# Optimization experiments

Measured on AMD Instinct MI355X. Metric: run time of the kernel, lower is better.

The kernel has to match this reference:

```python
import jax, jax.numpy as jnp
import numpy as np

V, D, H, E, C, K = 16000, 1024, 1024, 8, 16, 2  # vocab, embed, expert hidden, n_experts, classes, top_k
B, S = 64, 512
GATE_H = 256


def setup_inputs() -> dict:
    key = jax.random.key(0)
    ks = jax.random.split(key, 11)
    s = lambda i, shape: jax.random.normal(ks[i], shape, jnp.float32) * 0.02
    return dict(
        x=jax.random.randint(ks[0], (B, S), 0, V),
        emb=s(1, (V, D)),                      # shared gating embedding
        gate_w1=s(2, (D, GATE_H)), gate_b1=jnp.zeros((GATE_H,), jnp.float32),
        gate_w2=s(3, (GATE_H, E)), gate_b2=jnp.zeros((E,), jnp.float32),
        exp_emb=s(4, (E, V, D)),               # per-expert embedding tables
        exp_w1=s(5, (E, D, H)), exp_b1=jnp.zeros((E, H), jnp.float32),
        exp_w2=s(6, (E, H, C)), exp_b2=jnp.zeros((E, C), jnp.float32),
    )


def reference(x, emb, gate_w1, gate_b1, gate_w2, gate_b2,
              exp_emb, exp_w1, exp_b1, exp_w2, exp_b2):
    # --- gating: embed, mean-pool over seq, 2-layer MLP, softmax, top-k ---
    pooled = emb[x].mean(axis=1)                                   # [B,D]
    logits = jax.nn.relu(pooled @ gate_w1 + gate_b1) @ gate_w2 + gate_b2  # [B,E]
    probs = jax.nn.softmax(logits, axis=-1)
    rw, idx = jax.lax.top_k(probs, K)                              # [B,K]
    rw = rw / rw.sum(axis=-1, keepdims=True)                       # renormalize

    # --- dispatch: gather each sample's assigned expert params (no per-sample loop) ---
    out = jnp.zeros((x.shape[0], C), jnp.float32)
    for k in range(K):  # tiny fixed loop over top_k
        e = idx[:, k]                                              # [B]
        tok = exp_emb[e[:, None], x]                               # [B,S,D]
        h = jax.nn.relu(jnp.einsum('bsd,bdh->bsh', tok, exp_w1[e]) + exp_b1[e][:, None, :])  # [B,S,H]
        p = h.mean(axis=1)                                         # [B,H]
        eo = jnp.einsum('bh,bhc->bc', p, exp_w2[e]) + exp_b2[e]    # [B,C]
        out = out + rw[:, k:k + 1] * eo
    return out
```

## Files before the change

kernel.cpp:

```cpp
#include <hip/hip_runtime.h>
#include <hip/hip_bf16.h>

#define V_   16000
#define D_   1024
#define H_   1024
#define E_   8
#define C_   16
#define B_   64
#define S_   512
#define GH_  256
#define NPAIR 128

typedef short  bf16x8 __attribute__((ext_vector_type(8)));
typedef ushort u16x8  __attribute__((ext_vector_type(8)));
typedef float  f32x4  __attribute__((ext_vector_type(4)));

static __device__ __forceinline__ ushort f2bf(float f) {
  union { float f; unsigned u; } un; un.f = f;
  unsigned u = un.u;
  return (ushort)((u + 0x7FFFu + ((u >> 16) & 1u)) >> 16);
}

static __device__ __forceinline__ unsigned pk2(float lo, float hi) {
  __hip_bfloat162 h = __float22bfloat162_rn(make_float2(lo, hi));
  unsigned r; __builtin_memcpy(&r, &h, sizeof(r)); return r;
}

__global__ void prep_kernel(const float* __restrict__ w1, ushort* __restrict__ w1t,
                            const int* __restrict__ x, const float* __restrict__ emb,
                            float* __restrict__ partial) {
  __shared__ float tile[64][65];
  const int id = blockIdx.x;
  if (id < 2048) {
    const int e = id >> 8, rem = id & 255;
    const int dtile = rem & 15, htile = rem >> 4;
    const int d0 = dtile * 64, h0 = htile * 64;
    const float* src = w1 + (size_t)e * D_ * H_;
    for (int i = threadIdx.x; i < 64 * 64; i += 256) {
      int r = i >> 6, c = i & 63;
      tile[r][c] = src[(size_t)(d0 + r) * H_ + h0 + c];
    }
    __syncthreads();
    for (int i = threadIdx.x; i < 512; i += 256) {
      int chunk = i >> 6, lane = i & 63;
      int kkl = chunk >> 2, htl = chunk & 3;
      int l15 = lane & 15, l16 = lane >> 4;
      u16x8 v;
      #pragma unroll
      for (int j = 0; j < 8; ++j)
        v[j] = f2bf(tile[kkl * 32 + l16 * 8 + j][htl * 16 + l15]);
      size_t off = ((size_t)((e * 32 + dtile * 2 + kkl) * 64 + htile * 4 + htl)) * 512 + lane * 8;
      *reinterpret_cast<u16x8*>(w1t + off) = v;
    }
  } else {
    const int pid = id - 2048;
    const int b = pid >> 3, sb = pid & 7, t = threadIdx.x;
    const int* xr = x + b * S_ + sb * 64;
    float4 acc = make_float4(0.f, 0.f, 0.f, 0.f);
    #pragma unroll 4
    for (int s = 0; s < 64; ++s) {
      const float4* row = reinterpret_cast<const float4*>(emb + (size_t)xr[s] * D_);
      float4 v = row[t];
      acc.x += v.x; acc.y += v.y; acc.z += v.z; acc.w += v.w;
    }
    reinterpret_cast<float4*>(partial + ((size_t)b * 8 + sb) * D_)[t] = acc;
  }
}

__global__ void gate_kernel(const float* __restrict__ partial,
                            const float* __restrict__ gw1, const float* __restrict__ gb1,
                            const float* __restrict__ gw2, const float* __restrict__ gb2,
                            int* __restrict__ ridx, float* __restrict__ rwgt) {
  const int b = blockIdx.x, j = threadIdx.x;
  __shared__ float pl[D_];
  __shared__ float hid[GH_];
  __shared__ float logits[E_];
  for (int d = j; d < D_; d += 256) {
    float s = 0.f;
    #pragma unroll
    for (int sb = 0; sb < 8; ++sb) s += partial[((size_t)b * 8 + sb) * D_ + d];
    pl[d] = s * (1.f / (float)S_);
  }
  __syncthreads();
  float acc = gb1[j];
  for (int d = 0; d < D_; ++d) acc += pl[d] * gw1[d * GH_ + j];
  hid[j] = fmaxf(acc, 0.f);
  __syncthreads();
  if (j < E_) {
    float l = gb2[j];
    for (int i = 0; i < GH_; ++i) l += hid[i] * gw2[i * E_ + j];
    logits[j] = l;
  }
  __syncthreads();
  if (j == 0) {
    int i0 = 0; float v0 = logits[0];
    for (int i = 1; i < E_; ++i) if (logits[i] > v0) { v0 = logits[i]; i0 = i; }
    int i1 = -1; float v1 = -3.0e38f;
    for (int i = 0; i < E_; ++i) {
      if (i == i0) continue;
      if (logits[i] > v1) { v1 = logits[i]; i1 = i; }
    }
    float r1 = expf(v1 - v0);
    float norm = 1.f + r1;
    ridx[b * 2 + 0] = i0;         ridx[b * 2 + 1] = i1;
    rwgt[b * 2 + 0] = 1.f / norm; rwgt[b * 2 + 1] = r1 / norm;
  }
}

__global__ void sort_pairs_kernel(const int* __restrict__ ridx, int* __restrict__ order) {
  __shared__ int se[NPAIR];
  const int t = threadIdx.x;
  se[t] = ridx[t];
  __syncthreads();
  const int e = se[t];
  int rank = 0;
  for (int j = 0; j < NPAIR; ++j) {
    const int ej = se[j];
    rank += (ej < e || (ej == e && j < t)) ? 1 : 0;
  }
  order[rank] = t;
}

__global__ __launch_bounds__(512, 2) void expert_kernel(
    const int* __restrict__ x, const float* __restrict__ exp_emb,
    const ushort* __restrict__ w1t, const float* __restrict__ exp_b1,
    const int* __restrict__ ridx, const int* __restrict__ order,
    float* __restrict__ p_part) {
  const int id     = blockIdx.x;
  const int xcd    = id & 7;
  const int within = id >> 3;
  const int slot   = xcd * 128 + within;
  const int pr     = order[slot >> 3];
  const int sblk   = slot & 7;
  const int b      = pr >> 1;
  const int tid    = threadIdx.x;

  __shared__ __align__(16) ushort lB[64 * 1024];

  const int e = ridx[pr];

  const int grow = tid >> 3, gkq = (tid & 7) * 8;
  const int tok  = x[b * S_ + sblk * 64 + grow];
  const float* gptr = exp_emb + ((size_t)e * V_ + tok) * D_ + gkq;
  const int gdst = grow * 1024 + (gkq ^ ((grow & 7) << 3));

  const int wid = tid >> 6, lane = tid & 63;
  const int l15 = lane & 15, l16 = lane >> 4;
  const int sw  = (l15 & 7) << 3;

  const ushort* aW = w1t + (size_t)e * (32 * 64 * 512) + ((size_t)wid * 4) * 512 + (size_t)lane * 8;
  #define LOADA(t_, i_) \
    (*reinterpret_cast<const bf16x8*>(aW + ((size_t)(((t_) & 31) * 64 + ((t_) >> 5) * 32 + (i_))) * 512))

  f32x4 acc[4][4];
  #pragma unroll
  for (int i = 0; i < 4; ++i)
    #pragma unroll
    for (int j = 0; j < 4; ++j) acc[i][j] = (f32x4){0.f, 0.f, 0.f, 0.f};

  {
    f32x4 c0 = __builtin_nontemporal_load(reinterpret_cast<const f32x4*>(gptr));
    f32x4 c1 = __builtin_nontemporal_load(reinterpret_cast<const f32x4*>(gptr + 4));
    uint4 w;
    w.x = pk2(c0[0], c0[1]); w.y = pk2(c0[2], c0[3]);
    w.z = pk2(c1[0], c1[1]); w.w = pk2(c1[2], c1[3]);
    *reinterpret_cast<uint4*>(&lB[gdst]) = w;
  }

  bf16x8 af[4];
  #pragma unroll
  for (int i = 0; i < 4; ++i) af[i] = LOADA(0, i);

  #pragma unroll
  for (int slab = 0; slab < 16; ++slab) {
    __syncthreads();
    f32x4 n0, n1;
    if (slab < 15) {
      n0 = __builtin_nontemporal_load(reinterpret_cast<const f32x4*>(gptr + (slab + 1) * 64));
      n1 = __builtin_nontemporal_load(reinterpret_cast<const f32x4*>(gptr + (slab + 1) * 64 + 4));
    }
    #pragma unroll
    for (int ks = 0; ks < 2; ++ks) {
      const int kk = slab * 2 + ks;
      bf16x8 afn[4];
      #pragma unroll
      for (int i = 0; i < 4; ++i) afn[i] = LOADA(kk + 1, i);
      const int colk = (kk >> 1) * 64 + ((((kk & 1) << 5) | (l16 << 3)) ^ sw);
      bf16x8 bfr[4];
      #pragma unroll
      for (int j = 0; j < 4; ++j)
        bfr[j] = *reinterpret_cast<const bf16x8*>(&lB[(j * 16 + l15) * 1024 + colk]);
      #pragma unroll
      for (int i = 0; i < 4; ++i)
        #pragma unroll
        for (int j = 0; j < 4; ++j)
          acc[i][j] = __builtin_amdgcn_mfma_f32_16x16x32_bf16(af[i], bfr[j], acc[i][j], 0, 0, 0);
      #pragma unroll
      for (int i = 0; i < 4; ++i) af[i] = afn[i];
    }
    if (slab < 15) {
      uint4 w;
      w.x = pk2(n0[0], n0[1]); w.y = pk2(n0[2], n0[3]);
      w.z = pk2(n1[0], n1[1]); w.w = pk2(n1[2], n1[3]);
      *reinterpret_cast<uint4*>(&lB[gdst + (slab + 1) * 64]) = w;
    }
  }

  float* outRow = p_part + (size_t)(sblk * NPAIR + pr) * H_;
  const float* biasE = exp_b1 + e * H_;
  #pragma unroll
  for (int i = 0; i < 4; ++i) {
    #pragma unroll
    for (int r = 0; r < 4; ++r) {
      const int h = wid * 64 + i * 16 + l16 * 4 + r;
      const float bias = biasE[h];
      float v = 0.f;
      #pragma unroll
      for (int j = 0; j < 4; ++j) v += fmaxf(acc[i][j][r] + bias, 0.f);
      #pragma unroll
      for (int m = 1; m < 16; m <<= 1) v += __shfl_xor(v, m);
      if (l15 == 0) outRow[h] = v;
      acc[i][0][r] = 0.f;
    }
    #pragma unroll
    for (int j = 1; j < 4; ++j) acc[i][j] = (f32x4){0.f, 0.f, 0.f, 0.f};
  }

  #pragma unroll 4
  for (int t2 = 32; t2 < 64; ++t2) {
    bf16x8 afn[4];
    if (t2 < 63) {
      #pragma unroll
      for (int i = 0; i < 4; ++i) afn[i] = LOADA(t2 + 1, i);
    }
    const int kk = t2 - 32;
    const int colk = (kk >> 1) * 64 + ((((kk & 1) << 5) | (l16 << 3)) ^ sw);
    bf16x8 bfr[4];
    #pragma unroll
    for (int j = 0; j < 4; ++j)
      bfr[j] = *reinterpret_cast<const bf16x8*>(&lB[(j * 16 + l15) * 1024 + colk]);
    #pragma unroll
    for (int i = 0; i < 4; ++i)
      #pragma unroll
      for (int j = 0; j < 4; ++j)
        acc[i][j] = __builtin_amdgcn_mfma_f32_16x16x32_bf16(af[i], bfr[j], acc[i][j], 0, 0, 0);
    #pragma unroll
    for (int i = 0; i < 4; ++i) af[i] = afn[i];
  }

  #pragma unroll
  for (int i = 0; i < 4; ++i) {
    #pragma unroll
    for (int r = 0; r < 4; ++r) {
      const int h = 512 + wid * 64 + i * 16 + l16 * 4 + r;
      const float bias = biasE[h];
      float v = 0.f;
      #pragma unroll
      for (int j = 0; j < 4; ++j) v += fmaxf(acc[i][j][r] + bias, 0.f);
      #pragma unroll
      for (int m = 1; m < 16; m <<= 1) v += __shfl_xor(v, m);
      if (l15 == 0) outRow[h] = v;
    }
  }
  #undef LOADA
}

__global__ void finalize_kernel(const float* __restrict__ p_part,
                                const int* __restrict__ ridx, const float* __restrict__ rwgt,
                                const float* __restrict__ w2, const float* __restrict__ b2,
                                float* __restrict__ out) {
  const int b = blockIdx.x, t = threadIdx.x;
  const int c = t & 15, g = t >> 4;
  __shared__ float red[16][17];
  float res = 0.f;
  for (int kk = 0; kk < 2; ++kk) {
    const int pr = b * 2 + kk;
    const int e = ridx[pr];
    const float w = rwgt[pr];
    float dot = 0.f;
    for (int h = g; h < H_; h += 16) {
      float pm = 0.f;
      #pragma unroll
      for (int sb = 0; sb < 8; ++sb) pm += p_part[(size_t)(sb * NPAIR + pr) * H_ + h];
      dot += pm * w2[((size_t)e * H_ + h) * C_ + c];
    }
    red[g][c] = dot;
    __syncthreads();
    if (g == 0) {
      float s = 0.f;
      #pragma unroll
      for (int i = 0; i < 16; ++i) s += red[i][c];
      res += w * (s * (1.f / (float)S_) + b2[e * C_ + c]);
    }
    __syncthreads();
  }
  if (g == 0) out[b * C_ + c] = res;
}

extern "C" void kernel_launch(void* const* d_in, const int* in_sizes, int n_in,
                              void* d_out, int out_size, void* d_ws, size_t ws_size,
                              hipStream_t stream) {
  const int*   x    = (const int*)  d_in[0];
  const float* emb  = (const float*)d_in[1];
  const float* gw1  = (const float*)d_in[2];
  const float* gb1  = (const float*)d_in[3];
  const float* gw2  = (const float*)d_in[4];
  const float* gb2  = (const float*)d_in[5];
  const float* eemb = (const float*)d_in[6];
  const float* ew1  = (const float*)d_in[7];
  const float* eb1  = (const float*)d_in[8];
  const float* ew2  = (const float*)d_in[9];
  const float* eb2  = (const float*)d_in[10];
  float* out = (float*)d_out;

  char* ws = (char*)d_ws;
  const size_t OFF_W1T   = 0;
  const size_t OFF_PART  = (size_t)16 << 20;
  const size_t OFF_RIDX  = OFF_PART + ((size_t)2 << 20);
  const size_t OFF_RWGT  = OFF_RIDX + 1024;
  const size_t OFF_ORDER = OFF_RWGT + 1024;
  const size_t OFF_PPART = OFF_ORDER + 1024;

  ushort* w1t    = (ushort*)(ws + OFF_W1T);
  float*  part   = (float*) (ws + OFF_PART);
  int*    ridx   = (int*)   (ws + OFF_RIDX);
  float*  rwgt   = (float*) (ws + OFF_RWGT);
  int*    order  = (int*)   (ws + OFF_ORDER);
  float*  ppart  = (float*) (ws + OFF_PPART);

  prep_kernel<<<dim3(2560), 256, 0, stream>>>(ew1, w1t, x, emb, part);
  gate_kernel<<<dim3(B_), 256, 0, stream>>>(part, gw1, gb1, gw2, gb2, ridx, rwgt);
  sort_pairs_kernel<<<dim3(1), 128, 0, stream>>>(ridx, order);
  expert_kernel<<<dim3(1024), 512, 0, stream>>>(x, eemb, w1t, eb1, ridx, order, ppart);
  finalize_kernel<<<dim3(B_), 256, 0, stream>>>(ppart, ridx, rwgt, ew2, eb2, out);
}
```

Measured before the change: 301.6 us.

## Fuse both H halves into one K pass with 3-deep gather prefetch

The expert GEMM now processes both 512-wide H halves in a single sweep over K, keeping two accumulator sets (128 fp32 acc registers). The embedding gather is prefetched three slabs ahead in registers instead of one, and the barrier is replaced with an explicit lgkmcnt wait plus s_barrier placed after the LDS write. The aim is to overlap more of the global gather latency and remove the second LDS read pass over the tile. The cost is much higher register pressure, which may cut occupancy or cause spills, and the A-operand loads are no longer software-prefetched one step ahead.

```diff
diff --git a/kernel.cpp b/kernel.cpp
--- a/kernel.cpp
+++ b/kernel.cpp
@@ -24,6 +24,11 @@
 static __device__ __forceinline__ unsigned pk2(float lo, float hi) {
   __hip_bfloat162 h = __float22bfloat162_rn(make_float2(lo, hi));
   unsigned r; __builtin_memcpy(&r, &h, sizeof(r)); return r;
+}
+
+static __device__ __forceinline__ void bar_lgkm() {
+  asm volatile("s_waitcnt lgkmcnt(0)" ::: "memory");
+  __builtin_amdgcn_s_barrier();
 }
 
 __global__ void prep_kernel(const float* __restrict__ w1, ushort* __restrict__ w1t,
@@ -149,117 +154,86 @@
   const int sw  = (l15 & 7) << 3;
 
   const ushort* aW = w1t + (size_t)e * (32 * 64 * 512) + ((size_t)wid * 4) * 512 + (size_t)lane * 8;
-  #define LOADA(t_, i_) \
-    (*reinterpret_cast<const bf16x8*>(aW + ((size_t)(((t_) & 31) * 64 + ((t_) >> 5) * 32 + (i_))) * 512))
-
-  f32x4 acc[4][4];
+  #define LOADA(kk_, hh_, i_) \
+    (*reinterpret_cast<const bf16x8*>(aW + ((size_t)((kk_) * 64 + (hh_) * 32 + (i_))) * 512))
+
+  f32x4 acc[2][4][4];
   #pragma unroll
-  for (int i = 0; i < 4; ++i)
+  for (int hh = 0; hh < 2; ++hh)
     #pragma unroll
-    for (int j = 0; j < 4; ++j) acc[i][j] = (f32x4){0.f, 0.f, 0.f, 0.f};
-
+    for (int i = 0; i < 4; ++i)
+      #pragma unroll
+      for (int j = 0; j < 4; ++j) acc[hh][i][j] = (f32x4){0.f, 0.f, 0.f, 0.f};
+
+  f32x4 st[3][2];
+  #pragma unroll
+  for (int p = 0; p < 3; ++p) {
+    st[p][0] = __builtin_nontemporal_load(reinterpret_cast<const f32x4*>(gptr + p * 64));
+    st[p][1] = __builtin_nontemporal_load(reinterpret_cast<const f32x4*>(gptr + p * 64 + 4));
+  }
   {
-    f32x4 c0 = __builtin_nontemporal_load(reinterpret_cast<const f32x4*>(gptr));
-    f32x4 c1 = __builtin_nontemporal_load(reinterpret_cast<const f32x4*>(gptr + 4));
     uint4 w;
-    w.x = pk2(c0[0], c0[1]); w.y = pk2(c0[2], c0[3]);
-    w.z = pk2(c1[0], c1[1]); w.w = pk2(c1[2], c1[3]);
+    w.x = pk2(st[0][0][0], st[0][0][1]); w.y = pk2(st[0][0][2], st[0][0][3]);
+    w.z = pk2(st[0][1][0], st[0][1][1]); w.w = pk2(st[0][1][2], st[0][1][3]);
     *reinterpret_cast<uint4*>(&lB[gdst]) = w;
   }
-
-  bf16x8 af[4];
+  bar_lgkm();
+
   #pragma unroll
-  for (int i = 0; i < 4; ++i) af[i] = LOADA(0, i);
-
-  #pragma unroll
-  for (int slab = 0; slab < 16; ++slab) {
-    __syncthreads();
-    f32x4 n0, n1;
-    if (slab < 15) {
-      n0 = __builtin_nontemporal_load(reinterpret_cast<const f32x4*>(gptr + (slab + 1) * 64));
-      n1 = __builtin_nontemporal_load(reinterpret_cast<const f32x4*>(gptr + (slab + 1) * 64 + 4));
+  for (int s = 0; s < 16; ++s) {
+    if (s + 3 < 16) {
+      st[s % 3][0] = __builtin_nontemporal_load(reinterpret_cast<const f32x4*>(gptr + (s + 3) * 64));
+      st[s % 3][1] = __builtin_nontemporal_load(reinterpret_cast<const f32x4*>(gptr + (s + 3) * 64 + 4));
     }
     #pragma unroll
     for (int ks = 0; ks < 2; ++ks) {
-      const int kk = slab * 2 + ks;
-      bf16x8 afn[4];
-      #pragma unroll
-      for (int i = 0; i < 4; ++i) afn[i] = LOADA(kk + 1, i);
-      const int colk = (kk >> 1) * 64 + ((((kk & 1) << 5) | (l16 << 3)) ^ sw);
+      const int kk = s * 2 + ks;
+      const int colk = s * 64 + (((ks << 5) | (l16 << 3)) ^ sw);
       bf16x8 bfr[4];
       #pragma unroll
       for (int j = 0; j < 4; ++j)
         bfr[j] = *reinterpret_cast<const bf16x8*>(&lB[(j * 16 + l15) * 1024 + colk]);
+      bf16x8 af0[4], af1[4];
+      #pragma unroll
+      for (int i = 0; i < 4; ++i) { af0[i] = LOADA(kk, 0, i); af1[i] = LOADA(kk, 1, i); }
       #pragma unroll
       for (int i = 0; i < 4; ++i)
         #pragma unroll
         for (int j = 0; j < 4; ++j)
-          acc[i][j] = __builtin_amdgcn_mfma_f32_16x16x32_bf16(af[i], bfr[j], acc[i][j], 0, 0, 0);
-      #pragma unroll
-      for (int i = 0; i < 4; ++i) af[i] = afn[i];
-    }
-    if (slab < 15) {
+          acc[0][i][j] = __builtin_amdgcn_mfma_f32_16x16x32_bf16(af0[i], bfr[j], acc[0][i][j], 0, 0, 0);
+      #pragma unroll
+      for (int i = 0; i < 4; ++i)
+        #pragma unroll
+        for (int j = 0; j < 4; ++j)
+          acc[1][i][j] = __builtin_amdgcn_mfma_f32_16x16x32_bf16(af1[i], bfr[j], acc[1][i][j], 0, 0, 0);
+    }
+    if (s + 1 < 16) {
+      const int p = (s + 1) % 3;
       uint4 w;
-      w.x = pk2(n0[0], n0[1]); w.y = pk2(n0[2], n0[3]);
-      w.z = pk2(n1[0], n1[1]); w.w = pk2(n1[2], n1[3]);
-      *reinterpret_cast<uint4*>(&lB[gdst + (slab + 1) * 64]) = w;
-    }
+      w.x = pk2(st[p][0][0], st[p][0][1]); w.y = pk2(st[p][0][2], st[p][0][3]);
+      w.z = pk2(st[p][1][0], st[p][1][1]); w.w = pk2(st[p][1][2], st[p][1][3]);
+      *reinterpret_cast<uint4*>(&lB[gdst + (s + 1) * 64]) = w;
+    }
+    bar_lgkm();
   }
 
   float* outRow = p_part + (size_t)(sblk * NPAIR + pr) * H_;
   const float* biasE = exp_b1 + e * H_;
   #pragma unroll
-  for (int i = 0; i < 4; ++i) {
+  for (int hh = 0; hh < 2; ++hh) {
     #pragma unroll
-    for (int r = 0; r < 4; ++r) {
-      const int h = wid * 64 + i * 16 + l16 * 4 + r;
-      const float bias = biasE[h];
-      float v = 0.f;
-      #pragma unroll
-      for (int j = 0; j < 4; ++j) v += fmaxf(acc[i][j][r] + bias, 0.f);
-      #pragma unroll
-      for (int m = 1; m < 16; m <<= 1) v += __shfl_xor(v, m);
-      if (l15 == 0) outRow[h] = v;
-      acc[i][0][r] = 0.f;
-    }
-    #pragma unroll
-    for (int j = 1; j < 4; ++j) acc[i][j] = (f32x4){0.f, 0.f, 0.f, 0.f};
-  }
-
-  #pragma unroll 4
-  for (int t2 = 32; t2 < 64; ++t2) {
-    bf16x8 afn[4];
-    if (t2 < 63) {
-      #pragma unroll
-      for (int i = 0; i < 4; ++i) afn[i] = LOADA(t2 + 1, i);
-    }
-    const int kk = t2 - 32;
-    const int colk = (kk >> 1) * 64 + ((((kk & 1) << 5) | (l16 << 3)) ^ sw);
-    bf16x8 bfr[4];
-    #pragma unroll
-    for (int j = 0; j < 4; ++j)
-      bfr[j] = *reinterpret_cast<const bf16x8*>(&lB[(j * 16 + l15) * 1024 + colk]);
-    #pragma unroll
-    for (int i = 0; i < 4; ++i)
-      #pragma unroll
-      for (int j = 0; j < 4; ++j)
-        acc[i][j] = __builtin_amdgcn_mfma_f32_16x16x32_bf16(af[i], bfr[j], acc[i][j], 0, 0, 0);
-    #pragma unroll
-    for (int i = 0; i < 4; ++i) af[i] = afn[i];
-  }
-
-  #pragma unroll
-  for (int i = 0; i < 4; ++i) {
-    #pragma unroll
-    for (int r = 0; r < 4; ++r) {
-      const int h = 512 + wid * 64 + i * 16 + l16 * 4 + r;
-      const float bias = biasE[h];
-      float v = 0.f;
-      #pragma unroll
-      for (int j = 0; j < 4; ++j) v += fmaxf(acc[i][j][r] + bias, 0.f);
-      #pragma unroll
-      for (int m = 1; m < 16; m <<= 1) v += __shfl_xor(v, m);
-      if (l15 == 0) outRow[h] = v;
+    for (int i = 0; i < 4; ++i) {
+      #pragma unroll
+      for (int r = 0; r < 4; ++r) {
+        const int h = hh * 512 + wid * 64 + i * 16 + l16 * 4 + r;
+        const float bias = biasE[h];
+        float v = 0.f;
+        #pragma unroll
+        for (int j = 0; j < 4; ++j) v += fmaxf(acc[hh][i][j][r] + bias, 0.f);
+        #pragma unroll
+        for (int m = 1; m < 16; m <<= 1) v += __shfl_xor(v, m);
+        if (l15 == 0) outRow[h] = v;
+      }
     }
   }
   #undef LOADA
```

Result: slower. 317.8 us (+5.4%).
